# Optimization experiments

Hardware: AMD Instinct MI355X
Metric: run time of the kernel (lower is better)

## Reference

```python
import jax, jax.numpy as jnp
from jax import lax
import numpy as np

V, T, K, R, H, EN, L = 10000, 100, 50, 300, 200, 800, 3
B = 128
TRAIN_SIZE = 100000
DELTA = 0.005


def setup_inputs():
    key = jax.random.key(0)
    ks = jax.random.split(key, 16)
    s = 0.02
    return {
        "bows": jax.random.uniform(ks[0], (B, V), jnp.float32) * 10.0 + 1e-3,
        "times": jax.random.randint(ks[1], (B,), 0, T),
        "rnn_inp": jax.random.uniform(ks[2], (T, V), jnp.float32),
        "rho_W": jax.random.normal(ks[3], (V, R), jnp.float32) * s,
        "mu_q_alpha": jax.random.normal(ks[4], (K, T, R), jnp.float32),
        "logsigma_q_alpha": jax.random.normal(ks[5], (K, T, R), jnp.float32) * 0.1 - 2.0,
        "qtheta_W1": jax.random.normal(ks[6], (EN, V + K), jnp.float32) * s,
        "qtheta_b1": jnp.zeros((EN,), jnp.float32),
        "qtheta_W2": jax.random.normal(ks[7], (EN, EN), jnp.float32) * s,
        "qtheta_b2": jnp.zeros((EN,), jnp.float32),
        "mu_theta_W": jax.random.normal(ks[8], (K, EN), jnp.float32) * s,
        "mu_theta_b": jnp.zeros((K,), jnp.float32),
        "ls_theta_W": jax.random.normal(ks[9], (K, EN), jnp.float32) * s,
        "ls_theta_b": jnp.zeros((K,), jnp.float32),
        "eta_map_W": jax.random.normal(ks[10], (H, V), jnp.float32) * s,
        "eta_map_b": jnp.zeros((H,), jnp.float32),
        "lstm_Wih": jax.random.normal(ks[11], (L, 4 * H, H), jnp.float32) * s,
        "lstm_Whh": jax.random.normal(ks[12], (L, 4 * H, H), jnp.float32) * s,
        "lstm_bih": jnp.zeros((L, 4 * H), jnp.float32),
        "lstm_bhh": jnp.zeros((L, 4 * H), jnp.float32),
        "mu_eta_W": jax.random.normal(ks[13], (K, H + K), jnp.float32) * s,
        "mu_eta_b": jnp.zeros((K,), jnp.float32),
        "ls_eta_W": jax.random.normal(ks[14], (K, H + K), jnp.float32) * s,
        "ls_eta_b": jnp.zeros((K,), jnp.float32),
    }


def _kl(q_mu, q_ls, p_mu, p_ls):
    # KL(N(q_mu, exp(q_ls)) || N(p_mu, exp(p_ls))), logsigma == log-variance as in torch code
    return 0.5 * jnp.sum((jnp.exp(q_ls) + (q_mu - p_mu) ** 2) / (jnp.exp(p_ls) + 1e-6) - 1.0 + p_ls - q_ls, axis=-1)


def _lstm(x, Wih, Whh, bih, bhh):
    # x: [T, H]; L stacked LSTM layers (batch of 1 squeezed), torch gate order i,f,g,o
    for l in range(Wih.shape[0]):
        Wi, Wh, bi, bh = Wih[l], Whh[l], bih[l], bhh[l]
        Hd = Wh.shape[1]

        def step(carry, xt, Wi=Wi, Wh=Wh, bi=bi, bh=bh):
            h, c = carry
            g = Wi @ xt + Wh @ h + bi + bh
            i, f, gg, o = jnp.split(g, 4)
            c = jax.nn.sigmoid(f) * c + jax.nn.sigmoid(i) * jnp.tanh(gg)
            h = jax.nn.sigmoid(o) * jnp.tanh(c)
            return (h, c), h

        z = jnp.zeros((Hd,), x.dtype)
        _, x = lax.scan(step, (z, z), x)
    return x


def _forward(bows, rnn_inp, rho_W, mu_q_alpha, logsigma_q_alpha, qtheta_W1, qtheta_b1, qtheta_W2, qtheta_b2, mu_theta_W, mu_theta_b, ls_theta_W, ls_theta_b, eta_map_W, eta_map_b, lstm_Wih, lstm_Whh, lstm_bih, lstm_bhh, mu_eta_W, mu_eta_b, ls_eta_W, ls_eta_b, times):
    log_delta = jnp.log(jnp.float32(DELTA))
    # --- eta: LSTM over word-freq sequence, then sequential mu/logsigma/KL per t ---
    out = _lstm(rnn_inp @ eta_map_W.T + eta_map_b, lstm_Wih, lstm_Whh, lstm_bih, lstm_bhh)  # [T,H]
    p_ls_seq = jnp.concatenate([jnp.zeros((1,), jnp.float32), jnp.full((T - 1,), log_delta, jnp.float32)])

    def eta_step(eta_prev, xs):
        o_t, p_ls = xs
        x = jnp.concatenate([o_t, eta_prev])
        mu = mu_eta_W @ x + mu_eta_b
        ls = ls_eta_W @ x + ls_eta_b
        kl = _kl(mu, ls, eta_prev, jnp.full_like(mu, p_ls))
        return mu, (mu, kl)  # eval-mode reparameterize -> eta_t = mu

    _, (etas, kls) = lax.scan(eta_step, jnp.zeros((K,), jnp.float32), (out, p_ls_seq))
    kl_eta = kls.sum()
    # --- theta encoder ---
    nb = bows / bows.sum(1, keepdims=True)
    eta_td = etas[times]  # [B,K]
    h = jax.nn.relu(jnp.concatenate([nb, eta_td], axis=1) @ qtheta_W1.T + qtheta_b1)
    h = jax.nn.relu(h @ qtheta_W2.T + qtheta_b2)
    mu_t = h @ mu_theta_W.T + mu_theta_b
    ls_t = h @ ls_theta_W.T + ls_theta_b
    theta = jax.nn.softmax(mu_t, axis=-1)  # z = mu (eval-mode reparam)
    coeff = jnp.float32(TRAIN_SIZE / bows.shape[0])
    kl_theta = _kl(mu_t, ls_t, eta_td, jnp.zeros_like(mu_t)).sum() * coeff
    # --- alpha: with eval-mode reparam, alphas == mu, so KL is fully vectorized ---
    muT = jnp.transpose(mu_q_alpha, (1, 0, 2))  # [T,K,R]
    lsT = jnp.transpose(logsigma_q_alpha, (1, 0, 2))
    alphas = muT
    p_mu = jnp.concatenate([jnp.zeros((1, K, R), muT.dtype), alphas[:-1]], axis=0)
    p_ls = jnp.concatenate([jnp.zeros((1, K, R), muT.dtype), jnp.full((T - 1, K, R), log_delta, muT.dtype)], axis=0)
    kl_alpha = _kl(muT, lsT, p_mu, p_ls).sum()
    # --- beta and NLL ---
    logit = alphas.reshape(T * K, R) @ rho_W.T  # [T*K, V]
    beta = jax.nn.softmax(logit, axis=-1).reshape(T, K, V)
    beta_d = beta[times]  # [B,K,V]
    loglik = jnp.log(jnp.einsum('bk,bkv->bv', theta, beta_d) + 1e-12)
    nll = (-(loglik * bows).sum(-1)).sum() * coeff
    loss = nll + kl_eta + kl_theta + kl_alpha
    return loss, nll, kl_eta, kl_theta, kl_alpha


def reference(bows, times, rnn_inp, rho_W, mu_q_alpha, logsigma_q_alpha, qtheta_W1, qtheta_b1, qtheta_W2, qtheta_b2, mu_theta_W, mu_theta_b, ls_theta_W, ls_theta_b, eta_map_W, eta_map_b, lstm_Wih, lstm_Whh, lstm_bih, lstm_bhh, mu_eta_W, mu_eta_b, ls_eta_W, ls_eta_b):
    return _forward(bows, rnn_inp, rho_W, mu_q_alpha, logsigma_q_alpha, qtheta_W1, qtheta_b1, qtheta_W2, qtheta_b2, mu_theta_W, mu_theta_b, ls_theta_W, ls_theta_b, eta_map_W, eta_map_b, lstm_Wih, lstm_Whh, lstm_bih, lstm_bhh, mu_eta_W, mu_eta_b, ls_eta_W, ls_eta_b, times)
```

## Files before the change

kernel.cpp:

```cpp
#include <hip/hip_runtime.h>


typedef unsigned int u32;
typedef unsigned short u16;
typedef _Float16 f16;
typedef f16 f16x2 __attribute__((ext_vector_type(2)));
typedef short bf16x8 __attribute__((ext_vector_type(8)));
typedef float f32x4 __attribute__((ext_vector_type(4)));
typedef u32 u32x4 __attribute__((ext_vector_type(4)));

#define LOG_DELTA (-5.2983174f)
#define COEFF 781.25f

#if defined(__has_builtin)
#if __has_builtin(__builtin_amdgcn_sdot4)
#define HAVE_SDOT4 1
#endif
#endif

__device__ __forceinline__ float bf2f(u16 a) { return __uint_as_float(((u32)a) << 16); }
__device__ __forceinline__ u16 f2bf(float f) {
  u32 u = __float_as_uint(f);
  u32 r = (u + 0x7fffu + ((u >> 16) & 1u)) >> 16;
  return (u16)r;
}
__device__ __forceinline__ int dot4i8(u32 a, u32 b, int c) {
#ifdef HAVE_SDOT4
  return __builtin_amdgcn_sdot4(a, b, c, false);
#else
  int s = c;
  s += ((int)(a << 24) >> 24) * ((int)(b << 24) >> 24);
  s += ((int)(a << 16) >> 24) * ((int)(b << 16) >> 24);
  s += ((int)(a << 8) >> 24) * ((int)(b << 8) >> 24);
  s += ((int)a >> 24) * ((int)b >> 24);
  return s;
#endif
}
__device__ __forceinline__ float sigm(float x) { return 1.f / (1.f + __expf(-x)); }
__device__ __forceinline__ float ftanh(float x) { float t = __expf(2.f * x); return (t - 1.f) / (t + 1.f); }
__device__ __forceinline__ u16 f2h(float x) { return __builtin_bit_cast(u16, (f16)x); }
__device__ __forceinline__ float h2f(u16 x) { return (float)__builtin_bit_cast(f16, x); }
__device__ __forceinline__ void async_load16(const u16* g, u16* l) {
  __builtin_amdgcn_global_load_lds((const __attribute__((address_space(1))) u32*)g,
                                   (__attribute__((address_space(3))) u32*)l, 16, 0, 0);
}


__global__ __launch_bounds__(256) void k_init(
    const float* __restrict__ bih, const float* __restrict__ bhh, float* __restrict__ bsum,
    const float* __restrict__ muthb, const float* __restrict__ lsthb, float* __restrict__ mul,
    const float* __restrict__ muq, const float* __restrict__ lsq, float* __restrict__ alphapart,
    const float* __restrict__ mueb, const float* __restrict__ lseb, float* __restrict__ bias2e,
    float* __restrict__ accum) {
  const int bx = blockIdx.x, tid = threadIdx.x;
  if (bx < 10) {
    int i = bx * 256 + tid;
    if (i < 2400) bsum[i] = bih[i] + bhh[i];
    return;
  }
  if (bx == 10) {
    if (tid < 8) accum[tid] = 0.f;
    return;
  }
  if (bx < 523) {
    __shared__ float red[256];
    float s = 0.f;
    for (int i = (bx - 11) * 256 + tid; i < 1500000; i += 512 * 256) {
      int r = i % 300;
      int tk = i / 300;
      int k = tk % 50;
      int t = tk / 50;
      size_t idx = (size_t)k * 30000 + (size_t)t * 300 + r;
      float mu = muq[idx], ls = lsq[idx];
      float pm = 0.f, pls = 0.f;
      if (t > 0) { pm = muq[idx - 300]; pls = LOG_DELTA; }
      float d = mu - pm;
      s += 0.5f * ((__expf(ls) + d * d) / (__expf(pls) + 1e-6f) - 1.f + pls - ls);
    }
    red[tid] = s; __syncthreads();
    for (int o = 128; o > 0; o >>= 1) { if (tid < o) red[tid] += red[tid + o]; __syncthreads(); }
    if (tid == 0) alphapart[bx - 11] = red[0];
    return;
  }
  if (bx < 573) {
    int i = (bx - 523) * 256 + tid;
    if (i < 12800) { int c = i % 100; mul[i] = (c < 50) ? muthb[c] : lsthb[c - 50]; }
    return;
  }
  {
    if (tid < 100) bias2e[tid] = (tid < 50) ? mueb[tid] : lseb[tid - 50];
  }
}


__global__ __launch_bounds__(256) void k_nbquant(
    const float* __restrict__ bows, float* __restrict__ nb,
    const float* __restrict__ Whh, u32* __restrict__ whq, float* __restrict__ rowscale) {
  const int tid = threadIdx.x;
  if (blockIdx.x < 128) {
    __shared__ float red[256];
    const int b = blockIdx.x;
    float s = 0.f;
    for (int v = tid; v < 10000; v += 256) s += bows[b * 10000 + v];
    red[tid] = s; __syncthreads();
    for (int o = 128; o > 0; o >>= 1) { if (tid < o) red[tid] += red[tid + o]; __syncthreads(); }
    const float inv = 1.f / red[0];
    for (int v = tid; v < 10000; v += 256) nb[b * 10000 + v] = bows[b * 10000 + v] * inv;
    return;
  }
  __shared__ float wrow[4][200];
  const int wave = tid >> 6, lane = tid & 63;
  const int gr = (blockIdx.x - 128) * 4 + wave;
  const float* src = Whh + (size_t)gr * 200;
  float m = 0.f;
  for (int c = lane; c < 200; c += 64) { float v = src[c]; wrow[wave][c] = v; m = fmaxf(m, fabsf(v)); }
  for (int o = 32; o > 0; o >>= 1) m = fmaxf(m, __shfl_down(m, o));
  m = __shfl(m, 0);
  const float qs = (m > 0.f) ? 127.f / m : 0.f;
  const int l = gr / 800, rr = gr - l * 800;
  if (lane < 52) {
    u32 d = 0;
    if (lane < 50) {
#pragma unroll
      for (int b = 0; b < 4; ++b) {
        int q = __float2int_rn(wrow[wave][lane * 4 + b] * qs);
        q = max(-127, min(127, q));
        d |= ((u32)(q & 0xff)) << (8 * b);
      }
    }
    whq[l * 41600 + rr * 52 + lane] = d;
  }
  if (lane == 0) rowscale[gr] = (m > 0.f) ? m / 127.f : 0.f;
}


__global__ __launch_bounds__(256) void k_prepAB(const float* __restrict__ muq,
                                                const float* __restrict__ rho,
                                                u16* __restrict__ Abf, u16* __restrict__ Bbf) {
  if (blockIdx.x < 6400) {
    int idx = blockIdx.x * 256 + threadIdx.x;
    if (idx >= 5120 * 320) return;
    int r = idx % 320, m = idx / 320;
    float v = 0.f;
    if (r < 300 && m < 5000) { int t = m / 50, k = m - t * 50; v = muq[k * 30000 + t * 300 + r]; }
    Abf[idx] = f2bf(v);
    return;
  }
  int idx = (blockIdx.x - 6400) * 256 + threadIdx.x;
  if (idx >= 10112 * 320) return;
  int r = idx % 320, n = idx / 320;
  float v = (r < 300 && n < 10000) ? rho[n * 300 + r] : 0.f;
  Bbf[idx] = f2bf(v);
}


#define ST 64
#define SBK 32

template<int AMODE, int BMODE, int EPI>
__global__ __launch_bounds__(256) void gemm64(
    const float* __restrict__ A, const float* __restrict__ Bm, const float* __restrict__ Bm2,
    const float* __restrict__ bias, float* __restrict__ C,
    int M, int N, int Kd, int lda, int ldb,
    const int* __restrict__ times, const float* __restrict__ etas)
{
  __shared__ __align__(16) float As[SBK][ST + 4];
  __shared__ __align__(16) float Bs[SBK][ST + 4];
  const int tid = threadIdx.x;
  const int tx = tid & 15, ty = tid >> 4;
  const int m_base = blockIdx.x * ST, n_base = blockIdx.y * ST;
  float acc[4][4] = {};
  const int nkt = (Kd + SBK - 1) / SBK;
  const int per = (nkt + gridDim.z - 1) / gridDim.z;
  const int kt0 = blockIdx.z * per;
  const int kt1 = min(nkt, kt0 + per);
  const int lkk = tid & 31;
  const int lrow = tid >> 5;
  for (int kt = kt0; kt < kt1; ++kt) {
    const int kg = kt * SBK + lkk;
#pragma unroll
    for (int i = 0; i < 8; ++i) {
      const int m = m_base + lrow + i * 8;
      float v = 0.f;
      if (m < M && kg < Kd) {
        if (AMODE == 0) v = A[(size_t)m * lda + kg];
        else {
          if (kg < 10000) v = A[(size_t)m * 10000 + kg];
          else v = etas[times[m] * 50 + (kg - 10000)];
        }
      }
      As[lkk][lrow + i * 8] = v;
    }
#pragma unroll
    for (int i = 0; i < 8; ++i) {
      const int n = n_base + lrow + i * 8;
      float v = 0.f;
      if (n < N && kg < Kd) {
        if (BMODE == 0) v = Bm[(size_t)n * ldb + kg];
        else v = (n < 50) ? Bm[(size_t)n * ldb + kg] : Bm2[(size_t)(n - 50) * ldb + kg];
      }
      Bs[lkk][lrow + i * 8] = v;
    }
    __syncthreads();
#pragma unroll
    for (int kk = 0; kk < SBK; ++kk) {
      const float4 a4 = *(const float4*)&As[kk][ty * 4];
      const float4 b4 = *(const float4*)&Bs[kk][tx * 4];
      const float av[4] = {a4.x, a4.y, a4.z, a4.w};
      const float bv[4] = {b4.x, b4.y, b4.z, b4.w};
#pragma unroll
      for (int i = 0; i < 4; ++i)
#pragma unroll
        for (int j = 0; j < 4; ++j) acc[i][j] += av[i] * bv[j];
    }
    __syncthreads();
  }
#pragma unroll
  for (int i = 0; i < 4; ++i) {
    const int m = m_base + ty * 4 + i;
    if (m >= M) continue;
#pragma unroll
    for (int j = 0; j < 4; ++j) {
      const int n = n_base + tx * 4 + j;
      if (n >= N) continue;
      float v = acc[i][j];
      if (EPI == 1) { C[(size_t)m * N + n] = v + bias[n]; }
      else if (EPI == 2) { v += bias[n]; C[(size_t)m * N + n] = v > 0.f ? v : 0.f; }
      else if (EPI == 5) { atomicAdd(&C[(size_t)m * N + n], v); }
      else { C[(size_t)m * N + n] = v; }
    }
  }
}


#define LT 128
#define LBK 32

template<int AMODE>
__global__ __launch_bounds__(256) void gemm128p(
    const float* __restrict__ A, const float* __restrict__ Bm,
    float* __restrict__ P,
    int M, int N, int Kd, int lda, int ldb,
    const int* __restrict__ times, const float* __restrict__ etas)
{
  __shared__ __align__(16) float As[LBK][LT + 4];
  __shared__ __align__(16) float Bs[LBK][LT + 4];
  const int tid = threadIdx.x;
  const int tx = tid & 15, ty = tid >> 4;
  const int m_base = blockIdx.x * LT, n_base = blockIdx.y * LT;
  const int nkt = (Kd + LBK - 1) / LBK;
  const int per = (nkt + gridDim.z - 1) / gridDim.z;
  const int kt0 = blockIdx.z * per;
  const int kt1 = min(nkt, kt0 + per);
  const int lkk = tid & 31;
  const int lrow = tid >> 5;
  float acc[8][8] = {};
  float pa[16], pb[16];
  {
    const int kg = kt0 * LBK + lkk;
#pragma unroll
    for (int i = 0; i < 16; ++i) {
      const int m = m_base + lrow + i * 8;
      float v = 0.f;
      if (m < M && kg < Kd) {
        if (AMODE == 0) v = A[(size_t)m * lda + kg];
        else v = (kg < 10000) ? A[(size_t)m * 10000 + kg] : etas[times[m] * 50 + (kg - 10000)];
      }
      pa[i] = v;
      const int n = n_base + lrow + i * 8;
      float w = 0.f;
      if (n < N && kg < Kd) w = Bm[(size_t)n * ldb + kg];
      pb[i] = w;
    }
  }
  for (int kt = kt0; kt < kt1; ++kt) {
#pragma unroll
    for (int i = 0; i < 16; ++i) {
      As[lkk][lrow + i * 8] = pa[i];
      Bs[lkk][lrow + i * 8] = pb[i];
    }
    __syncthreads();
    if (kt + 1 < kt1) {
      const int kg = (kt + 1) * LBK + lkk;
#pragma unroll
      for (int i = 0; i < 16; ++i) {
        const int m = m_base + lrow + i * 8;
        float v = 0.f;
        if (m < M && kg < Kd) {
          if (AMODE == 0) v = A[(size_t)m * lda + kg];
          else v = (kg < 10000) ? A[(size_t)m * 10000 + kg] : etas[times[m] * 50 + (kg - 10000)];
        }
        pa[i] = v;
        const int n = n_base + lrow + i * 8;
        float w = 0.f;
        if (n < N && kg < Kd) w = Bm[(size_t)n * ldb + kg];
        pb[i] = w;
      }
    }
#pragma unroll
    for (int kk = 0; kk < LBK; ++kk) {
      const float4* ap = (const float4*)&As[kk][ty * 8];
      const float4* bp = (const float4*)&Bs[kk][tx * 8];
      const float4 a0 = ap[0], a1 = ap[1];
      const float4 b0 = bp[0], b1 = bp[1];
      const float av[8] = {a0.x, a0.y, a0.z, a0.w, a1.x, a1.y, a1.z, a1.w};
      const float bv[8] = {b0.x, b0.y, b0.z, b0.w, b1.x, b1.y, b1.z, b1.w};
#pragma unroll
      for (int i = 0; i < 8; ++i)
#pragma unroll
        for (int j = 0; j < 8; ++j) acc[i][j] += av[i] * bv[j];
    }
    __syncthreads();
  }
  float* Cz = P + (size_t)blockIdx.z * M * N;
#pragma unroll
  for (int i = 0; i < 8; ++i) {
    const int m = m_base + ty * 8 + i;
    if (m >= M) continue;
#pragma unroll
    for (int j = 0; j < 8; ++j) {
      const int n = n_base + tx * 8 + j;
      if (n >= N) continue;
      Cz[(size_t)m * N + n] = acc[i][j];
    }
  }
}

template<int EPI>
__global__ __launch_bounds__(256) void k_reduceZ(const float* __restrict__ P,
                                                 const float* __restrict__ bias,
                                                 float* __restrict__ out,
                                                 int N, int total, int Z) {
  for (int i = blockIdx.x * 256 + threadIdx.x; i < total; i += gridDim.x * 256) {
    float s = bias[i % N];
    for (int z = 0; z < Z; ++z) s += P[(size_t)z * total + i];
    if (EPI == 2) s = s > 0.f ? s : 0.f;
    out[i] = s;
  }
}


__global__ __launch_bounds__(256) void gemm_mfma_bT(
    const u16* __restrict__ A, const u16* __restrict__ B, u16* __restrict__ C,
    int M, int N)
{
  __shared__ u16 As[128 * 32];
  __shared__ u16 Bs[128 * 32];
  const int tid = threadIdx.x;
  const int l = tid & 63, w = tid >> 6;
  const int wm = w & 1, wn = w >> 1;
  const int m0 = blockIdx.x * 128, n0 = blockIdx.y * 128;
  f32x4 acc[4][4] = {};
  const int arow = l >> 2;
  const int acol = (l & 3) * 8;
  for (int kt = 0; kt < 10; ++kt) {
    const int k0 = kt * 32;
#pragma unroll
    for (int c = 0; c < 2; ++c) {
      const int i = w + c * 4;
      async_load16(A + (size_t)(m0 + i * 16 + arow) * 320 + k0 + acol, As + i * 512);
      async_load16(B + (size_t)(n0 + i * 16 + arow) * 320 + k0 + acol, Bs + i * 512);
    }
    __syncthreads();
    bf16x8 af[4], bfr[4];
#pragma unroll
    for (int x = 0; x < 4; ++x) {
      af[x]  = *(const bf16x8*)&As[(wm * 64 + x * 16 + (l & 15)) * 32 + (l >> 4) * 8];
      bfr[x] = *(const bf16x8*)&Bs[(wn * 64 + x * 16 + (l & 15)) * 32 + (l >> 4) * 8];
    }
#pragma unroll
    for (int x = 0; x < 4; ++x)
#pragma unroll
      for (int y = 0; y < 4; ++y)
        acc[x][y] = __builtin_amdgcn_mfma_f32_16x16x32_bf16(af[x], bfr[y], acc[x][y], 0, 0, 0);
    __syncthreads();
  }
  const int col = l & 15, quad = l >> 4;
#pragma unroll
  for (int x = 0; x < 4; ++x) {
    const int gmB = m0 + wm * 64 + x * 16 + quad * 4;
#pragma unroll
    for (int y = 0; y < 4; ++y) {
      const int gn = n0 + wn * 64 + y * 16 + col;
      if (gn >= N) continue;
#pragma unroll
      for (int r = 0; r < 4; ++r) {
        const int gm = gmB + r;
        if (gm < M) C[(size_t)gm * N + gn] = f2bf(acc[x][y][r]);
      }
    }
  }
}


__global__ __launch_bounds__(512, 1) void lstm_scan_reg(
    const u32* __restrict__ whq,
    const float* __restrict__ rowscale,
    const float* __restrict__ xproj,
    float* __restrict__ hseq)
{
  __shared__ u16 pg[800];
  __shared__ __align__(16) u32 hq[52];
  __shared__ float wmax[8];
  __shared__ float hscale_s[1];
  const int tid = threadIdx.x;
  const int act = (tid < 400);
  const int rA = act ? tid : 399;
  const u32x4* gA = (const u32x4*)(whq + (size_t)rA * 52);
  const u32x4* gB = (const u32x4*)(whq + (size_t)(rA + 400) * 52);
  u32x4 wA4[13], wB4[13];
#pragma unroll
  for (int i = 0; i < 13; ++i) { wA4[i] = gA[i]; wB4[i] = gB[i]; }
  float rsA = 0.f, rsB = 0.f, xpA = 0.f, xpB = 0.f;
  if (act) {
    rsA = rowscale[tid]; rsB = rowscale[tid + 400];
    xpA = xproj[tid]; xpB = xproj[tid + 400];
  }
  if (tid < 52) hq[tid] = 0;
  if (tid < 8) wmax[tid] = 0.f;
  if (tid == 0) hscale_s[0] = 0.f;
  float c_reg = 0.f;
  __syncthreads();
  for (int t = 0; t < 100; ++t) {
    if (act) {
      float nxA = 0.f, nxB = 0.f;
      if (t < 99) { nxA = xproj[(t + 1) * 800 + tid]; nxB = xproj[(t + 1) * 800 + tid + 400]; }
      const float hdq = hscale_s[0];
      u32x4 hv4[13];
#pragma unroll
      for (int i = 0; i < 13; ++i) hv4[i] = *((const u32x4*)hq + i);
      int aA = 0, aB = 0;
#pragma unroll
      for (int g = 0; g < 50; ++g) {
        const u32 h = hv4[g >> 2][g & 3];
        aA = dot4i8(wA4[g >> 2][g & 3], h, aA);
        aB = dot4i8(wB4[g >> 2][g & 3], h, aB);
      }
      pg[tid] = f2h((float)aA * (rsA * hdq) + xpA);
      pg[tid + 400] = f2h((float)aB * (rsB * hdq) + xpB);
      xpA = nxA; xpB = nxB;
    }
    __syncthreads();
    float hv = 0.f;
    if (tid < 200) {
      float gi = sigm(h2f(pg[tid]));
      float gf = sigm(h2f(pg[200 + tid]));
      float gg = ftanh(h2f(pg[400 + tid]));
      float go = sigm(h2f(pg[600 + tid]));
      c_reg = gf * c_reg + gi * gg;
      hv = go * ftanh(c_reg);
      hseq[t * 200 + tid] = hv;
    }
    float m = fabsf(hv);
    for (int o = 32; o > 0; o >>= 1) m = fmaxf(m, __shfl_down(m, o));
    if ((tid & 63) == 0) wmax[tid >> 6] = m;
    __syncthreads();
    if (tid < 200) {
      const float hm = fmaxf(fmaxf(wmax[0], wmax[1]), fmaxf(wmax[2], wmax[3]));
      const float qs = (hm > 0.f) ? 127.f / hm : 0.f;
      int q = __float2int_rn(hv * qs);
      q = max(-127, min(127, q));
      ((signed char*)hq)[tid] = (signed char)q;
      if (tid == 0) hscale_s[0] = (hm > 0.f) ? hm / 127.f : 0.f;
    }
    __syncthreads();
  }
}


__global__ __launch_bounds__(64, 1) void eta_scan_reg(
    const float* __restrict__ muW, const float* __restrict__ lsW,
    const float* __restrict__ pc0,
    float* __restrict__ etas, float* __restrict__ accum)
{
  __shared__ __align__(16) float ep[52];
  const int j = threadIdx.x;
  const int act = (j < 50);
  float wmu[52], wls[52];
  if (act) {
#pragma unroll
    for (int k = 0; k < 25; ++k) {
      float2 a = *(const float2*)(muW + (size_t)j * 250 + 200 + 2 * k);
      float2 b = *(const float2*)(lsW + (size_t)j * 250 + 200 + 2 * k);
      wmu[2 * k] = a.x; wmu[2 * k + 1] = a.y;
      wls[2 * k] = b.x; wls[2 * k + 1] = b.y;
    }
    wmu[50] = wmu[51] = wls[50] = wls[51] = 0.f;
  } else {
#pragma unroll
    for (int k = 0; k < 52; ++k) { wmu[k] = 0.f; wls[k] = 0.f; }
  }
  if (j < 52) ep[j] = 0.f;
  float klacc = 0.f;
  float mye = 0.f;
  float pmu = act ? pc0[j] : 0.f;
  float pls_ = act ? pc0[50 + j] : 0.f;
  __syncthreads();
  for (int t = 0; t < 100; ++t) {
    float nmu = 0.f, nls = 0.f;
    if (act && t < 99) { nmu = pc0[(t + 1) * 100 + j]; nls = pc0[(t + 1) * 100 + 50 + j]; }
    float ma[4] = {pmu, 0.f, 0.f, 0.f};
    float la[4] = {pls_, 0.f, 0.f, 0.f};
    const float4* e4 = (const float4*)ep;
#pragma unroll
    for (int i = 0; i < 13; ++i) {
      const float4 e = e4[i];
      ma[0] += wmu[4 * i + 0] * e.x; ma[1] += wmu[4 * i + 1] * e.y;
      ma[2] += wmu[4 * i + 2] * e.z; ma[3] += wmu[4 * i + 3] * e.w;
      la[0] += wls[4 * i + 0] * e.x; la[1] += wls[4 * i + 1] * e.y;
      la[2] += wls[4 * i + 2] * e.z; la[3] += wls[4 * i + 3] * e.w;
    }
    const float mu = (ma[0] + ma[1]) + (ma[2] + ma[3]);
    const float ls = (la[0] + la[1]) + (la[2] + la[3]);
    __syncthreads();
    if (act) {
      const float pls = (t == 0) ? 0.f : LOG_DELTA;
      const float pv = __expf(pls) + 1e-6f;
      const float d = mu - mye;
      klacc += 0.5f * ((__expf(ls) + d * d) / pv - 1.f + pls - ls);
      etas[t * 50 + j] = mu;
      mye = mu;
      ep[j] = mu;
    }
    __syncthreads();
    pmu = nmu; pls_ = nls;
  }
  for (int o = 32; o > 0; o >>= 1) klacc += __shfl_down(klacc, o);
  if (j == 0) accum[0] = klacc;
}


__global__ __launch_bounds__(64) void k_theta(const float* __restrict__ mul,
                                              const float* __restrict__ etas, const int* __restrict__ times,
                                              float* __restrict__ theta, float* __restrict__ accum) {
  const int b = blockIdx.x, lane = threadIdx.x;
  float m_ = 0.f, l_ = 0.f, e_ = 0.f, mx = -1e30f;
  if (lane < 50) {
    m_ = mul[b * 100 + lane];
    l_ = mul[b * 100 + 50 + lane];
    e_ = etas[times[b] * 50 + lane];
    mx = m_;
  }
  for (int o = 32; o > 0; o >>= 1) mx = fmaxf(mx, __shfl_down(mx, o));
  mx = __shfl(mx, 0);
  float ex = (lane < 50) ? __expf(m_ - mx) : 0.f;
  float sum = ex;
  for (int o = 32; o > 0; o >>= 1) sum += __shfl_down(sum, o);
  sum = __shfl(sum, 0);
  if (lane < 50) theta[b * 50 + lane] = ex / sum;
  float kl = 0.f;
  if (lane < 50) {
    float d = m_ - e_;
    kl = 0.5f * ((__expf(l_) + d * d) / (1.f + 1e-6f) - 1.f - l_);
  }
  for (int o = 32; o > 0; o >>= 1) kl += __shfl_down(kl, o);
  if (lane == 0) atomicAdd(accum + 1, kl);
}


__global__ __launch_bounds__(256) void k_rowsum(const u16* __restrict__ logit, float* __restrict__ Z) {
  const int r = blockIdx.x, tid = threadIdx.x;
  const u32* row = (const u32*)(logit + (size_t)r * 10000);
  __shared__ float red[256];
  float s = 0.f;
  for (int v = tid; v < 5000; v += 256) {
    u32 p = row[v];
    s += __expf(bf2f((u16)(p & 0xffffu))) + __expf(bf2f((u16)(p >> 16)));
  }
  red[tid] = s; __syncthreads();
  for (int o = 128; o > 0; o >>= 1) { if (tid < o) red[tid] += red[tid + o]; __syncthreads(); }
  if (tid == 0) Z[r] = red[0];
}


__global__ __launch_bounds__(256) void k_nll(const u16* __restrict__ logit, const float* __restrict__ Z,
                                             const float* __restrict__ theta, const float* __restrict__ bows,
                                             const int* __restrict__ times, float* __restrict__ accum) {
  const int b = blockIdx.x, seg = blockIdx.y, tid = threadIdx.x;
  const int t = times[b];
  __shared__ float c2[52];
  __shared__ float red[256];
  if (tid < 50) c2[tid] = theta[b * 50 + tid] / Z[t * 50 + tid];
  __syncthreads();
  float part = 0.f;
  const int v0 = seg * 1250, v1 = v0 + 1250;
  const u16* base = logit + (size_t)t * 500000;
  for (int v = v0 + tid; v < v1; v += 256) {
    float ssv = 1e-12f;
#pragma unroll
    for (int k = 0; k < 50; ++k) ssv += c2[k] * __expf(bf2f(base[k * 10000 + v]));
    part += bows[b * 10000 + v] * __logf(ssv);
  }
  red[tid] = part; __syncthreads();
  for (int o = 128; o > 0; o >>= 1) { if (tid < o) red[tid] += red[tid + o]; __syncthreads(); }
  if (tid == 0) atomicAdd(accum + 3, -red[0]);
}


__global__ __launch_bounds__(64) void k_final(const float* __restrict__ accum,
                                              const float* __restrict__ alphapart,
                                              float* __restrict__ out) {
  const int tid = threadIdx.x;
  float s = 0.f;
  for (int i = tid; i < 512; i += 64) s += alphapart[i];
  for (int o = 32; o > 0; o >>= 1) s += __shfl_down(s, o);
  if (tid == 0) {
    float nll = accum[3] * COEFF;
    float kl_eta = accum[0];
    float kl_theta = accum[1] * COEFF;
    float kl_alpha = s;
    out[0] = nll + kl_eta + kl_theta + kl_alpha;
    out[1] = nll;
    out[2] = kl_eta;
    out[3] = kl_theta;
    out[4] = kl_alpha;
  }
}


extern "C" void kernel_launch(void* const* d_in, const int* in_sizes, int n_in,
                              void* d_out, int out_size, void* d_ws, size_t ws_size,
                              hipStream_t stream) {
  (void)in_sizes; (void)n_in; (void)out_size; (void)ws_size;
  const float* bows   = (const float*)d_in[0];
  const int*   times  = (const int*)d_in[1];
  const float* rnn_in = (const float*)d_in[2];
  const float* rho_W  = (const float*)d_in[3];
  const float* muq    = (const float*)d_in[4];
  const float* lsq    = (const float*)d_in[5];
  const float* qW1    = (const float*)d_in[6];
  const float* qb1    = (const float*)d_in[7];
  const float* qW2    = (const float*)d_in[8];
  const float* qb2    = (const float*)d_in[9];
  const float* muthW  = (const float*)d_in[10];
  const float* muthb  = (const float*)d_in[11];
  const float* lsthW  = (const float*)d_in[12];
  const float* lsthb  = (const float*)d_in[13];
  const float* emW    = (const float*)d_in[14];
  const float* emb    = (const float*)d_in[15];
  const float* Wih    = (const float*)d_in[16];
  const float* Whh    = (const float*)d_in[17];
  const float* bih    = (const float*)d_in[18];
  const float* bhh    = (const float*)d_in[19];
  const float* mueW   = (const float*)d_in[20];
  const float* mueb   = (const float*)d_in[21];
  const float* lseW   = (const float*)d_in[22];
  const float* lseb   = (const float*)d_in[23];
  float* out = (float*)d_out;
  float* ws = (float*)d_ws;

  float* accum = ws + 0;
  float* nb    = ws + 8;
  float* x0    = ws + 1280008;
  float* xproj = ws + 1300008;
  float* hsA   = ws + 1380008;
  float* hsB   = ws + 1400008;
  u32*   whq   = (u32*)(ws + 1420008);
  float* rowsc = ws + 1544808;
  float* bias2e= ws + 1547208;
  float* pc0   = ws + 1547408;
  float* alphp = ws + 1558008;
  float* hsC   = ws + 1560008;
  float* bsum  = ws + 1660008;
  float* etas  = ws + 1662408;
  float* h1    = ws + 1667408;
  float* h2    = ws + 1769808;
  float* mul   = ws + 1872208;
  float* theta = ws + 1885008;
  float* Zrow  = ws + 1891408;
  u16*   A_bf  = (u16*)(ws + 1896408);
  u16*   B_bf  = (u16*)(ws + 2715608);
  u16*   logit = (u16*)(ws + 4333528);
  float* P1    = ws + 4333528;
  float* Px0   = ws + 8941528;
  float* P2    = ws + 10221528;

  k_init<<<574, 256, 0, stream>>>(bih, bhh, bsum, muthb, lsthb, mul,
                                  muq, lsq, alphp, mueb, lseb, bias2e, accum);
  k_nbquant<<<728, 256, 0, stream>>>(bows, nb, Whh, whq, rowsc);
  k_prepAB<<<19040, 256, 0, stream>>>(muq, rho_W, A_bf, B_bf);

  gemm128p<0><<<dim3(1, 2, 64), 256, 0, stream>>>(rnn_in, emW, Px0,
                                                  100, 200, 10000, 10000, 10000, nullptr, nullptr);
  k_reduceZ<1><<<79, 256, 0, stream>>>(Px0, emb, x0, 200, 20000, 64);

  const float* lin[3] = {x0, hsA, hsB};
  float* lout[3] = {hsA, hsB, hsC};
  for (int l = 0; l < 3; ++l) {
    gemm64<0, 0, 1><<<dim3(2, 13, 1), 256, 0, stream>>>(lin[l], Wih + l * 160000, nullptr,
                                                        bsum + l * 800, xproj,
                                                        100, 800, 200, 200, 200, nullptr, nullptr);
    lstm_scan_reg<<<1, 512, 0, stream>>>(whq + l * 41600, rowsc + l * 800, xproj, lout[l]);
  }
  gemm64<0, 1, 1><<<dim3(2, 2, 1), 256, 0, stream>>>(hsC, mueW, lseW, bias2e, pc0,
                                                     100, 100, 200, 200, 250, nullptr, nullptr);
  eta_scan_reg<<<1, 64, 0, stream>>>(mueW, lseW, pc0, etas, accum);

  gemm128p<2><<<dim3(1, 7, 45), 256, 0, stream>>>(nb, qW1, P1,
                                                  128, 800, 10050, 10000, 10050, times, etas);
  k_reduceZ<2><<<400, 256, 0, stream>>>(P1, qb1, h1, 800, 102400, 45);
  gemm128p<0><<<dim3(1, 7, 5), 256, 0, stream>>>(h1, qW2, P2,
                                                 128, 800, 800, 800, 800, nullptr, nullptr);
  k_reduceZ<2><<<400, 256, 0, stream>>>(P2, qb2, h2, 800, 102400, 5);
  gemm64<0, 1, 5><<<dim3(2, 2, 5), 256, 0, stream>>>(h2, muthW, lsthW, nullptr, mul,
                                                     128, 100, 800, 800, 800, nullptr, nullptr);
  k_theta<<<128, 64, 0, stream>>>(mul, etas, times, theta, accum);

  gemm_mfma_bT<<<dim3(40, 79), 256, 0, stream>>>(A_bf, B_bf, logit, 5000, 10000);
  k_rowsum<<<5000, 256, 0, stream>>>(logit, Zrow);
  k_nll<<<dim3(128, 8), 256, 0, stream>>>(logit, Zrow, theta, bows, times, accum);

  k_final<<<1, 64, 0, stream>>>(accum, alphp, out);
}
```

Baseline: 1.127 ms.

## Stage quantized LSTM recurrent weights in LDS with transposed interleaved layout

The quantized Whh is now written transposed, as [dword][row], instead of row-major padded to 52 dwords. The LSTM scan kernel copies the first 48 dword-columns (about 150KB) into LDS once, keeps the last two columns in registers, and reads adjacent row pairs with 8-byte LDS loads. It also changes which gate rows each thread owns from (tid, tid+400) to (2tid, 2tid+1). The aim is to cut the register pressure of keeping 104 weight dwords per thread, at the cost of LDS reads in every timestep of the serial loop and a large LDS footprint. Workspace offsets shrink to match the removed padding.

```diff
diff --git a/kernel.cpp b/kernel.cpp
--- a/kernel.cpp
+++ b/kernel.cpp
@@ -8,6 +8,7 @@
 typedef short bf16x8 __attribute__((ext_vector_type(8)));
 typedef float f32x4 __attribute__((ext_vector_type(4)));
 typedef u32 u32x4 __attribute__((ext_vector_type(4)));
+typedef u32 u32x2 __attribute__((ext_vector_type(2)));
 
 #define LOG_DELTA (-5.2983174f)
 #define COEFF 781.25f
@@ -118,17 +119,15 @@
   m = __shfl(m, 0);
   const float qs = (m > 0.f) ? 127.f / m : 0.f;
   const int l = gr / 800, rr = gr - l * 800;
-  if (lane < 52) {
+  if (lane < 50) {
     u32 d = 0;
-    if (lane < 50) {
-#pragma unroll
-      for (int b = 0; b < 4; ++b) {
-        int q = __float2int_rn(wrow[wave][lane * 4 + b] * qs);
-        q = max(-127, min(127, q));
-        d |= ((u32)(q & 0xff)) << (8 * b);
-      }
-    }
-    whq[l * 41600 + rr * 52 + lane] = d;
+#pragma unroll
+    for (int b = 0; b < 4; ++b) {
+      int q = __float2int_rn(wrow[wave][lane * 4 + b] * qs);
+      q = max(-127, min(127, q));
+      d |= ((u32)(q & 0xff)) << (8 * b);
+    }
+    whq[l * 40000 + lane * 800 + rr] = d;
   }
   if (lane == 0) rowscale[gr] = (m > 0.f) ? m / 127.f : 0.f;
 }
@@ -393,28 +392,27 @@
 }
 
 
-__global__ __launch_bounds__(512, 1) void lstm_scan_reg(
+__global__ __launch_bounds__(512, 1) void lstm_scan_lds2(
     const u32* __restrict__ whq,
     const float* __restrict__ rowscale,
     const float* __restrict__ xproj,
     float* __restrict__ hseq)
 {
+  __shared__ __align__(16) u32 WL[38400];
   __shared__ u16 pg[800];
   __shared__ __align__(16) u32 hq[52];
   __shared__ float wmax[8];
   __shared__ float hscale_s[1];
   const int tid = threadIdx.x;
   const int act = (tid < 400);
-  const int rA = act ? tid : 399;
-  const u32x4* gA = (const u32x4*)(whq + (size_t)rA * 52);
-  const u32x4* gB = (const u32x4*)(whq + (size_t)(rA + 400) * 52);
-  u32x4 wA4[13], wB4[13];
-#pragma unroll
-  for (int i = 0; i < 13; ++i) { wA4[i] = gA[i]; wB4[i] = gB[i]; }
+  const int tca = act ? tid : 399;
+  for (int i = tid; i < 38400; i += 512) WL[i] = whq[i];
+  const u32 w48A = whq[38400 + 2 * tca], w48B = whq[38400 + 2 * tca + 1];
+  const u32 w49A = whq[39200 + 2 * tca], w49B = whq[39200 + 2 * tca + 1];
   float rsA = 0.f, rsB = 0.f, xpA = 0.f, xpB = 0.f;
   if (act) {
-    rsA = rowscale[tid]; rsB = rowscale[tid + 400];
-    xpA = xproj[tid]; xpB = xproj[tid + 400];
+    rsA = rowscale[2 * tid]; rsB = rowscale[2 * tid + 1];
+    xpA = xproj[2 * tid]; xpB = xproj[2 * tid + 1];
   }
   if (tid < 52) hq[tid] = 0;
   if (tid < 8) wmax[tid] = 0.f;
@@ -424,20 +422,33 @@
   for (int t = 0; t < 100; ++t) {
     if (act) {
       float nxA = 0.f, nxB = 0.f;
-      if (t < 99) { nxA = xproj[(t + 1) * 800 + tid]; nxB = xproj[(t + 1) * 800 + tid + 400]; }
+      if (t < 99) { nxA = xproj[(t + 1) * 800 + 2 * tid]; nxB = xproj[(t + 1) * 800 + 2 * tid + 1]; }
       const float hdq = hscale_s[0];
-      u32x4 hv4[13];
-#pragma unroll
-      for (int i = 0; i < 13; ++i) hv4[i] = *((const u32x4*)hq + i);
+      const u32x4* hq4c = (const u32x4*)hq;
+      const u32x4 h0 = hq4c[0], h1 = hq4c[1], h2 = hq4c[2], h3 = hq4c[3];
+      const u32x4 h4 = hq4c[4], h5 = hq4c[5], h6 = hq4c[6], h7 = hq4c[7];
+      const u32x4 h8 = hq4c[8], h9 = hq4c[9], h10 = hq4c[10], h11 = hq4c[11];
+      const u32x4 h12 = hq4c[12];
       int aA = 0, aB = 0;
-#pragma unroll
-      for (int g = 0; g < 50; ++g) {
-        const u32 h = hv4[g >> 2][g & 3];
-        aA = dot4i8(wA4[g >> 2][g & 3], h, aA);
-        aB = dot4i8(wB4[g >> 2][g & 3], h, aB);
-      }
-      pg[tid] = f2h((float)aA * (rsA * hdq) + xpA);
-      pg[tid + 400] = f2h((float)aB * (rsB * hdq) + xpB);
+#define D2(d, hh) { const u32x2 w = *(const u32x2*)(WL + (d) * 800 + 2 * tca); \
+      aA = dot4i8(w.x, (hh), aA); aB = dot4i8(w.y, (hh), aB); }
+      D2(0, h0.x)  D2(1, h0.y)  D2(2, h0.z)  D2(3, h0.w)
+      D2(4, h1.x)  D2(5, h1.y)  D2(6, h1.z)  D2(7, h1.w)
+      D2(8, h2.x)  D2(9, h2.y)  D2(10, h2.z) D2(11, h2.w)
+      D2(12, h3.x) D2(13, h3.y) D2(14, h3.z) D2(15, h3.w)
+      D2(16, h4.x) D2(17, h4.y) D2(18, h4.z) D2(19, h4.w)
+      D2(20, h5.x) D2(21, h5.y) D2(22, h5.z) D2(23, h5.w)
+      D2(24, h6.x) D2(25, h6.y) D2(26, h6.z) D2(27, h6.w)
+      D2(28, h7.x) D2(29, h7.y) D2(30, h7.z) D2(31, h7.w)
+      D2(32, h8.x) D2(33, h8.y) D2(34, h8.z) D2(35, h8.w)
+      D2(36, h9.x) D2(37, h9.y) D2(38, h9.z) D2(39, h9.w)
+      D2(40, h10.x) D2(41, h10.y) D2(42, h10.z) D2(43, h10.w)
+      D2(44, h11.x) D2(45, h11.y) D2(46, h11.z) D2(47, h11.w)
+#undef D2
+      aA = dot4i8(w48A, h12.x, aA); aB = dot4i8(w48B, h12.x, aB);
+      aA = dot4i8(w49A, h12.y, aA); aB = dot4i8(w49B, h12.y, aB);
+      pg[2 * tid] = f2h((float)aA * (rsA * hdq) + xpA);
+      pg[2 * tid + 1] = f2h((float)aB * (rsB * hdq) + xpB);
       xpA = nxA; xpB = nxB;
     }
     __syncthreads();
@@ -656,10 +667,10 @@
   float* hsA   = ws + 1380008;
   float* hsB   = ws + 1400008;
   u32*   whq   = (u32*)(ws + 1420008);
-  float* rowsc = ws + 1544808;
-  float* bias2e= ws + 1547208;
-  float* pc0   = ws + 1547408;
-  float* alphp = ws + 1558008;
+  float* rowsc = ws + 1540008;
+  float* bias2e= ws + 1542408;
+  float* pc0   = ws + 1542608;
+  float* alphp = ws + 1552608;
   float* hsC   = ws + 1560008;
   float* bsum  = ws + 1660008;
   float* etas  = ws + 1662408;
@@ -690,7 +701,7 @@
     gemm64<0, 0, 1><<<dim3(2, 13, 1), 256, 0, stream>>>(lin[l], Wih + l * 160000, nullptr,
                                                         bsum + l * 800, xproj,
                                                         100, 800, 200, 200, 200, nullptr, nullptr);
-    lstm_scan_reg<<<1, 512, 0, stream>>>(whq + l * 41600, rowsc + l * 800, xproj, lout[l]);
+    lstm_scan_lds2<<<1, 512, 0, stream>>>(whq + l * 40000, rowsc + l * 800, xproj, lout[l]);
   }
   gemm64<0, 1, 1><<<dim3(2, 2, 1), 256, 0, stream>>>(hsC, mueW, lseW, bias2e, pc0,
                                                      100, 100, 200, 200, 250, nullptr, nullptr);
```

Measured after the change: 1.230 ms. 1.09x slower.
